# Kernel optimization log

Hardware: AMD Instinct MI355X
Metric: run time of the kernel (lower is better)

The kernel has to match this reference:

```python
import jax, jax.numpy as jnp
import numpy as np

N_NODES = 100000
N_EDGES = 3200000
IN_Z = 32
PROJ_H = 64
LOOP_D = 32
DEC_H = 64


def setup_inputs() -> dict:
    key = jax.random.key(0)
    ks = jax.random.split(key, 10)
    z_mod = jax.random.normal(ks[0], (N_NODES, IN_Z), dtype=jnp.float32)
    edge_index = jax.random.randint(ks[1], (2, N_EDGES), 0, N_NODES, dtype=jnp.int64)
    # loop_proj: Linear(32->64), ReLU, Linear(64->32)
    w1 = jax.random.normal(ks[2], (IN_Z, PROJ_H), dtype=jnp.float32) / np.sqrt(IN_Z)
    b1 = jnp.zeros((PROJ_H,), dtype=jnp.float32)
    w2 = jax.random.normal(ks[3], (PROJ_H, LOOP_D), dtype=jnp.float32) / np.sqrt(PROJ_H)
    b2 = jnp.zeros((LOOP_D,), dtype=jnp.float32)
    # decoder: Linear(2*loop_dim -> dec_hidden), ReLU, Linear(dec_hidden -> 1)
    dw1 = jax.random.normal(ks[4], (2 * LOOP_D, DEC_H), dtype=jnp.float32) / np.sqrt(2 * LOOP_D)
    db1 = jnp.zeros((DEC_H,), dtype=jnp.float32)
    dw2 = jax.random.normal(ks[5], (DEC_H, 1), dtype=jnp.float32) / np.sqrt(DEC_H)
    db2 = jnp.zeros((1,), dtype=jnp.float32)
    return {"z_mod": z_mod, "edge_index": edge_index, "w1": w1, "b1": b1,
            "w2": w2, "b2": b2, "dw1": dw1, "db1": db1, "dw2": dw2, "db2": db2}


def reference(z_mod, edge_index, w1, b1, w2, b2, dw1, db1, dw2, db2):
    # loop_proj: z_mod -> z_loop  [N, loop_dim]
    h = jax.nn.relu(z_mod @ w1 + b1)
    z_loop = h @ w2 + b2
    # edge-wise decoder: gather, concat, MLP
    zi = z_loop[edge_index[0]]            # [E, loop_dim]
    zj = z_loop[edge_index[1]]            # [E, loop_dim]
    he = jnp.concatenate([zi, zj], axis=-1)  # [E, 2*loop_dim]
    he = jax.nn.relu(he @ dw1 + db1)         # [E, dec_hidden]
    logits = (he @ dw2 + db2)[..., 0]        # [E]
    return logits
```

## Files before the change

### kernel.cpp

```cpp
#include <hip/hip_runtime.h>


typedef short bfrag4 __attribute__((ext_vector_type(4)));
typedef short s16x8  __attribute__((ext_vector_type(8)));
typedef float f32x4v __attribute__((ext_vector_type(4)));

#define N_NODES 100000
#define N_EDGES 3200000

__device__ __forceinline__ unsigned short f2bf(float f) {
    unsigned int i = __float_as_uint(f);
    unsigned int r = i + 0x7FFFu + ((i >> 16) & 1u);
    return (unsigned short)(r >> 16);
}

__device__ __forceinline__ bfrag4 cvt4(float x0, float x1, float x2, float x3) {
    bfrag4 v;
    v[0] = (short)f2bf(x0);
    v[1] = (short)f2bf(x1);
    v[2] = (short)f2bf(x2);
    v[3] = (short)f2bf(x3);
    return v;
}

__global__ __launch_bounds__(256) void node_proj_kernel(
    const float* __restrict__ z_mod,
    const float* __restrict__ w1,
    const float* __restrict__ b1,
    const float* __restrict__ w2,
    const float* __restrict__ b2,
    unsigned short* __restrict__ z_loop)
{
    __shared__ unsigned short hbuf[4][16 * 72];

    const int tid  = threadIdx.x;
    const int wave = tid >> 6;
    const int lane = tid & 63;
    const int quad = lane >> 4;
    const int col  = lane & 15;

    bfrag4 bw1[2][4];
    float  bias1[4];
    for (int t = 0; t < 4; ++t) {
        const int n = col + 16 * t;
        for (int s = 0; s < 2; ++s)
            for (int j = 0; j < 4; ++j)
                bw1[s][t][j] = (short)f2bf(w1[(s * 16 + quad * 4 + j) * 64 + n]);
        bias1[t] = b1[n];
    }
    bfrag4 bw2[4][2];
    float  bias2[2];
    for (int t = 0; t < 2; ++t) {
        const int n = col + 16 * t;
        for (int s = 0; s < 4; ++s)
            for (int j = 0; j < 4; ++j)
                bw2[s][t][j] = (short)f2bf(w2[(s * 16 + quad * 4 + j) * 32 + n]);
        bias2[t] = b2[n];
    }

    unsigned short* hrow = &hbuf[wave][0];

    const int gwave  = blockIdx.x * 4 + wave;
    const int nwaves = gridDim.x * 4;
    const int ntiles = N_NODES / 16;

    for (int tile = gwave; tile < ntiles; tile += nwaves) {
        const int node0 = tile * 16;
        const float* zrow = z_mod + (size_t)(node0 + col) * 32;

        f32x4v za0 = *(const f32x4v*)(zrow + 0 * 16 + quad * 4);
        f32x4v za1 = *(const f32x4v*)(zrow + 1 * 16 + quad * 4);
        bfrag4 a10 = cvt4(za0[0], za0[1], za0[2], za0[3]);
        bfrag4 a11 = cvt4(za1[0], za1[1], za1[2], za1[3]);

        f32x4v acc[4];
        for (int t = 0; t < 4; ++t) {
            f32x4v c = {bias1[t], bias1[t], bias1[t], bias1[t]};
            c = __builtin_amdgcn_mfma_f32_16x16x16bf16_1k(a10, bw1[0][t], c, 0, 0, 0);
            c = __builtin_amdgcn_mfma_f32_16x16x16bf16_1k(a11, bw1[1][t], c, 0, 0, 0);
            acc[t] = c;
        }

        for (int t = 0; t < 4; ++t)
            for (int r = 0; r < 4; ++r) {
                float v = acc[t][r];
                v = v > 0.f ? v : 0.f;
                hrow[(quad * 4 + r) * 72 + (col + 16 * t)] = f2bf(v);
            }
        asm volatile("" ::: "memory");

        f32x4v acc2[2];
        for (int t = 0; t < 2; ++t)
            acc2[t] = (f32x4v){bias2[t], bias2[t], bias2[t], bias2[t]};
        for (int s = 0; s < 4; ++s) {
            bfrag4 a2 = *(const bfrag4*)(hrow + col * 72 + s * 16 + quad * 4);
            for (int t = 0; t < 2; ++t)
                acc2[t] = __builtin_amdgcn_mfma_f32_16x16x16bf16_1k(a2, bw2[s][t], acc2[t], 0, 0, 0);
        }
        asm volatile("" ::: "memory");

        for (int t = 0; t < 2; ++t)
            for (int r = 0; r < 4; ++r)
                z_loop[(size_t)(node0 + quad * 4 + r) * 32 + (col + 16 * t)] =
                    f2bf(acc2[t][r]);
    }
}

__global__ __launch_bounds__(256) void edge_dec_kernel(
    const int*            __restrict__ eidx,
    const unsigned short* __restrict__ z_loop,
    const float*          __restrict__ dw1,
    const float*          __restrict__ db1,
    const float*          __restrict__ dw2,
    const float*          __restrict__ db2,
    float* __restrict__ out)
{
    const int tid  = threadIdx.x;
    const int lane = tid & 63;
    const int quad = lane >> 4;
    const int col  = lane & 15;

    s16x8 aw[2][4];
    f32x4v bias1v[4];
    float  w2v[4][4];
    for (int mt = 0; mt < 4; ++mt) {
        const int h = 16 * mt + col;
        for (int s = 0; s < 2; ++s)
            for (int j = 0; j < 8; ++j)
                aw[s][mt][j] = (short)f2bf(dw1[(32 * s + quad * 8 + j) * 64 + h]);
        for (int r = 0; r < 4; ++r) {
            bias1v[mt][r] = db1[16 * mt + quad * 4 + r];
            w2v[mt][r]    = dw2[16 * mt + quad * 4 + r];
        }
    }
    const float bias2 = db2[0];

    const int gwave  = blockIdx.x * 4 + (tid >> 6);
    const int nwaves = gridDim.x * 4;
    const int npairs = N_EDGES / 32;

    const char* zbase = (const char*)z_loop;
    const char* ebase = (const char*)eidx;
    const int qoff  = quad * 16;
    const int colb  = col * 4;
    const int colb2 = N_EDGES * 4 + colb;

    int sA = *(const int*)(ebase + gwave * 128 + colb)       << 6;
    int sB = *(const int*)(ebase + gwave * 128 + 64 + colb)  << 6;
    int dA = *(const int*)(ebase + gwave * 128 + colb2)      << 6;
    int dB = *(const int*)(ebase + gwave * 128 + 64 + colb2) << 6;

    for (int p = gwave; p < npairs; p += nwaves) {
        const int e0 = p * 32;

        s16x8 gA0 = *(const s16x8*)(zbase + (sA + qoff));
        s16x8 gA1 = *(const s16x8*)(zbase + (dA + qoff));
        s16x8 gB0 = *(const s16x8*)(zbase + (sB + qoff));
        s16x8 gB1 = *(const s16x8*)(zbase + (dB + qoff));

        const int pn = p + nwaves;
        const int pb = (pn < npairs ? pn : gwave) * 128;
        sA = *(const int*)(ebase + pb + colb)       << 6;
        sB = *(const int*)(ebase + pb + 64 + colb)  << 6;
        dA = *(const int*)(ebase + pb + colb2)      << 6;
        dB = *(const int*)(ebase + pb + 64 + colb2) << 6;

        f32x4v accA[4], accB[4];
        for (int mt = 0; mt < 4; ++mt) {
            f32x4v c = __builtin_amdgcn_mfma_f32_16x16x32_bf16(aw[0][mt], gA0, bias1v[mt], 0, 0, 0);
            accA[mt] = __builtin_amdgcn_mfma_f32_16x16x32_bf16(aw[1][mt], gA1, c, 0, 0, 0);
        }
        for (int mt = 0; mt < 4; ++mt) {
            f32x4v c = __builtin_amdgcn_mfma_f32_16x16x32_bf16(aw[0][mt], gB0, bias1v[mt], 0, 0, 0);
            accB[mt] = __builtin_amdgcn_mfma_f32_16x16x32_bf16(aw[1][mt], gB1, c, 0, 0, 0);
        }

        float pA = 0.f, pB = 0.f;
        for (int mt = 0; mt < 4; ++mt)
            for (int r = 0; r < 4; ++r) {
                float vA = accA[mt][r]; vA = vA > 0.f ? vA : 0.f;
                float vB = accB[mt][r]; vB = vB > 0.f ? vB : 0.f;
                pA += vA * w2v[mt][r];
                pB += vB * w2v[mt][r];
            }
        pA += __shfl_xor(pA, 16, 64);
        pA += __shfl_xor(pA, 32, 64);
        pB += __shfl_xor(pB, 16, 64);
        pB += __shfl_xor(pB, 32, 64);

        if (lane < 32) {
            float v = (lane < 16 ? pA : pB) + bias2;
            out[e0 + lane] = v;
        }
    }
}

extern "C" void kernel_launch(void* const* d_in, const int* in_sizes, int n_in,
                              void* d_out, int out_size, void* d_ws, size_t ws_size,
                              hipStream_t stream) {
    const float* z_mod = (const float*)d_in[0];
    const int*   eidx  = (const int*)d_in[1];
    const float* w1    = (const float*)d_in[2];
    const float* b1    = (const float*)d_in[3];
    const float* w2    = (const float*)d_in[4];
    const float* b2    = (const float*)d_in[5];
    const float* dw1   = (const float*)d_in[6];
    const float* db1   = (const float*)d_in[7];
    const float* dw2   = (const float*)d_in[8];
    const float* db2   = (const float*)d_in[9];
    float*          out    = (float*)d_out;
    unsigned short* z_loop = (unsigned short*)d_ws;

    node_proj_kernel<<<512, 256, 0, stream>>>(z_mod, w1, b1, w2, b2, z_loop);
    edge_dec_kernel<<<2048, 256, 0, stream>>>(eidx, z_loop, dw1, db1, dw2, db2, out);
}
```

Baseline: 154.5 us.

## Double-buffer edge gathers through LDS with async global_load_lds prefetch

The edge decoder now gathers the node embeddings for the next edge tile straight into a per-wave LDS double buffer with global_load_lds. Each iteration reads the current tile from LDS and runs the MFMAs while the next tile's gathers are in flight, and edge indices are prefetched two iterations ahead. The grid shrinks from 2048 to 1280 blocks to suit the added 32KB of LDS per block. The goal is to hide gather latency behind compute. The cost is an s_waitcnt vmcnt(0) at the top of each iteration, which also waits on index and output traffic, and lower occupancy from the LDS use.

```diff
diff --git a/kernel.cpp b/kernel.cpp
--- a/kernel.cpp
+++ b/kernel.cpp
@@ -7,6 +7,11 @@
 
 #define N_NODES 100000
 #define N_EDGES 3200000
+
+#define GLDS16(gp, lp)                                                        \
+    __builtin_amdgcn_global_load_lds(                                         \
+        (const __attribute__((address_space(1))) unsigned int*)(gp),          \
+        (__attribute__((address_space(3))) unsigned int*)(lp), 16, 0, 0)
 
 __device__ __forceinline__ unsigned short f2bf(float f) {
     unsigned int i = __float_as_uint(f);
@@ -115,7 +120,10 @@
     const float*          __restrict__ db2,
     float* __restrict__ out)
 {
+    __shared__ char lbuf[4][2][4][1024];
+
     const int tid  = threadIdx.x;
+    const int wave = tid >> 6;
     const int lane = tid & 63;
     const int quad = lane >> 4;
     const int col  = lane & 15;
@@ -135,7 +143,7 @@
     }
     const float bias2 = db2[0];
 
-    const int gwave  = blockIdx.x * 4 + (tid >> 6);
+    const int gwave  = blockIdx.x * 4 + wave;
     const int nwaves = gridDim.x * 4;
     const int npairs = N_EDGES / 32;
 
@@ -145,25 +153,53 @@
     const int colb  = col * 4;
     const int colb2 = N_EDGES * 4 + colb;
 
+    char* myl = &lbuf[wave][0][0][0];
+    const int lslot = lane * 16;
+
     int sA = *(const int*)(ebase + gwave * 128 + colb)       << 6;
     int sB = *(const int*)(ebase + gwave * 128 + 64 + colb)  << 6;
     int dA = *(const int*)(ebase + gwave * 128 + colb2)      << 6;
     int dB = *(const int*)(ebase + gwave * 128 + 64 + colb2) << 6;
-
-    for (int p = gwave; p < npairs; p += nwaves) {
-        const int e0 = p * 32;
-
-        s16x8 gA0 = *(const s16x8*)(zbase + (sA + qoff));
-        s16x8 gA1 = *(const s16x8*)(zbase + (dA + qoff));
-        s16x8 gB0 = *(const s16x8*)(zbase + (sB + qoff));
-        s16x8 gB1 = *(const s16x8*)(zbase + (dB + qoff));
-
-        const int pn = p + nwaves;
+    GLDS16(zbase + (sA + qoff), myl + 0 * 1024);
+    GLDS16(zbase + (dA + qoff), myl + 1 * 1024);
+    GLDS16(zbase + (sB + qoff), myl + 2 * 1024);
+    GLDS16(zbase + (dB + qoff), myl + 3 * 1024);
+    {
+        const int pn = gwave + nwaves;
         const int pb = (pn < npairs ? pn : gwave) * 128;
         sA = *(const int*)(ebase + pb + colb)       << 6;
         sB = *(const int*)(ebase + pb + 64 + colb)  << 6;
         dA = *(const int*)(ebase + pb + colb2)      << 6;
         dB = *(const int*)(ebase + pb + 64 + colb2) << 6;
+    }
+
+    int cur = 0;
+    for (int p = gwave; p < npairs; p += nwaves) {
+        const int e0 = p * 32;
+
+        asm volatile("s_waitcnt vmcnt(0)" ::: "memory");
+
+        char* bcur = myl + cur * 4096;
+        char* bnxt = myl + (cur ^ 1) * 4096;
+
+        GLDS16(zbase + (sA + qoff), bnxt + 0 * 1024);
+        GLDS16(zbase + (dA + qoff), bnxt + 1 * 1024);
+        GLDS16(zbase + (sB + qoff), bnxt + 2 * 1024);
+        GLDS16(zbase + (dB + qoff), bnxt + 3 * 1024);
+
+        {
+            const int pn = p + 2 * nwaves;
+            const int pb = (pn < npairs ? pn : gwave) * 128;
+            sA = *(const int*)(ebase + pb + colb)       << 6;
+            sB = *(const int*)(ebase + pb + 64 + colb)  << 6;
+            dA = *(const int*)(ebase + pb + colb2)      << 6;
+            dB = *(const int*)(ebase + pb + 64 + colb2) << 6;
+        }
+
+        s16x8 gA0 = *(const s16x8*)(bcur + 0 * 1024 + lslot);
+        s16x8 gA1 = *(const s16x8*)(bcur + 1 * 1024 + lslot);
+        s16x8 gB0 = *(const s16x8*)(bcur + 2 * 1024 + lslot);
+        s16x8 gB1 = *(const s16x8*)(bcur + 3 * 1024 + lslot);
 
         f32x4v accA[4], accB[4];
         for (int mt = 0; mt < 4; ++mt) {
@@ -192,6 +228,8 @@
             float v = (lane < 16 ? pA : pB) + bias2;
             out[e0 + lane] = v;
         }
+
+        cur ^= 1;
     }
 }
 
@@ -212,5 +250,5 @@
     unsigned short* z_loop = (unsigned short*)d_ws;
 
     node_proj_kernel<<<512, 256, 0, stream>>>(z_mod, w1, b1, w2, b2, z_loop);
-    edge_dec_kernel<<<2048, 256, 0, stream>>>(eidx, z_loop, dw1, db1, dw2, db2, out);
-}
+    edge_dec_kernel<<<1280, 256, 0, stream>>>(eidx, z_loop, dw1, db1, dw2, db2, out);
+}
```

Measured after the change: 164.4 us. 6.4% more time.
